# Kernel optimization log

Hardware: AMD Instinct MI355X
Metric: run time of the kernel (lower is better)

The kernel has to match this reference:

```python
import jax, jax.numpy as jnp
import numpy as np

N_ATOMS, E_ATOMS, E_BONDS, N_FRAGS, E_FRAGS = 200000, 800000, 3200000, 20000, 60000
D, EB, H, DH = 128, 12, 3, 4  # atom dim, bond-node feat dim, n_heads, per-head dim (EB // H)


def _seg_softmax(logits, seg, num):
    # scatter_softmax over segments given by `seg` along axis 0
    m = jax.ops.segment_max(logits, seg, num_segments=num)
    m = jnp.where(jnp.isfinite(m), m, 0.0)  # guard empty segments
    e = jnp.exp(logits - m[seg])
    s = jax.ops.segment_sum(e, seg, num_segments=num)
    return e / s[seg]


def setup_inputs() -> dict:
    key = jax.random.key(0)
    ks = jax.random.split(key, 16)
    s = 0.05
    return dict(
        x_atoms=jax.random.normal(ks[0], (N_ATOMS, D), jnp.float32),
        edge_index=jax.random.randint(ks[1], (2, E_ATOMS), 0, N_ATOMS, jnp.int32),
        edge_attr=jax.random.normal(ks[2], (E_ATOMS, EB), jnp.float32),
        frag_index=jax.random.randint(ks[3], (2, E_FRAGS), 0, N_FRAGS, jnp.int32),
        x_frags=jax.random.normal(ks[4], (N_FRAGS, D), jnp.float32),
        atom_to_frag_ids=jax.random.randint(ks[5], (N_ATOMS,), 0, N_FRAGS, jnp.int32),
        node_features_bond_graph=jax.random.normal(ks[6], (E_ATOMS, EB), jnp.float32),
        edge_index_bonds_graph=jax.random.randint(ks[7], (2, E_BONDS), 0, E_ATOMS, jnp.int32),
        edge_attr_bond_graph=jax.random.normal(ks[8], (E_BONDS, 1), jnp.float32),
        W_atom=jax.random.normal(ks[9], (D, D), jnp.float32) * s,
        b_atom=jnp.zeros((D,), jnp.float32),
        W_edge=jax.random.normal(ks[10], (EB, D), jnp.float32) * s,
        b_edge=jnp.zeros((D,), jnp.float32),
        W_proj=jax.random.normal(ks[11], (EB, EB), jnp.float32) * s,
        b_proj=jnp.zeros((EB,), jnp.float32),
        a_b=jax.random.normal(ks[12], (H, 2 * DH + 1), jnp.float32) * s,
        W_f1=jax.random.normal(ks[13], (D, 2 * D), jnp.float32) * s,
        b_f1=jnp.zeros((2 * D,), jnp.float32),
        W_f2=jax.random.normal(ks[14], (2 * D, D), jnp.float32) * s,
        b_f2=jnp.zeros((D,), jnp.float32),
    )


def reference(x_atoms, edge_index, edge_attr, frag_index, x_frags, atom_to_frag_ids,
              node_features_bond_graph, edge_index_bonds_graph, edge_attr_bond_graph,
              W_atom, b_atom, W_edge, b_edge, W_proj, b_proj, a_b,
              W_f1, b_f1, W_f2, b_f2):
    Nb = node_features_bond_graph.shape[0]  # bond-graph nodes == atom-graph edges
    N = x_atoms.shape[0]
    Nf = x_frags.shape[0]

    # ---- GAT-style attention on the bond (line) graph ----
    tgt_b, src_b = edge_index_bonds_graph[0], edge_index_bonds_graph[1]
    nf = (node_features_bond_graph @ W_proj + b_proj).reshape(Nb, H, DH)
    tf = nf[tgt_b]                                  # [Eb, H, DH]
    sf = nf[src_b]                                  # [Eb, H, DH]
    ea = jnp.broadcast_to(edge_attr_bond_graph[:, None, :], (tgt_b.shape[0], H, 1))
    msg = jnp.concatenate([tf, ea, sf], axis=-1)    # [Eb, H, 2*DH+1]
    logits = jax.nn.leaky_relu(jnp.sum(msg * a_b, axis=2), 0.2)  # [Eb, H]
    attn = _seg_softmax(logits, tgt_b, Nb)
    agg = jax.ops.segment_sum(attn[..., None] * sf, tgt_b, num_segments=Nb)  # [Nb, H, DH]
    new_bond = agg.reshape(Nb, H * DH)              # [Nb, EB]

    # edge embedding (computed in the original forward; not used in returned outputs)
    edge_attr_full = jnp.concatenate(
        [new_bond, jnp.zeros((N, EB), edge_attr.dtype)], axis=0)
    _ = edge_attr_full @ W_edge + b_edge

    # ---- degree-normalized GCN propagation on atom graph with self loops ----
    x = x_atoms @ W_atom + b_atom
    loop = jnp.arange(N, dtype=edge_index.dtype)
    src = jnp.concatenate([edge_index[0], loop])
    tgt = jnp.concatenate([edge_index[1], loop])
    deg = jax.ops.segment_sum(jnp.ones(src.shape, x.dtype), src, num_segments=N)
    dinv = jnp.where(deg > 0, 1.0 / jnp.sqrt(jnp.maximum(deg, 1.0)), 0.0)
    norm = dinv[src] * dinv[tgt]
    x_new = jax.ops.segment_sum(x[src] * norm[:, None], tgt, num_segments=N)  # [N, D]

    # ---- fragment pooling + fragment-graph propagation ----
    frag_feat = jax.ops.segment_sum(x_new, atom_to_frag_ids, num_segments=Nf)  # [Nf, D]
    fs, ft = frag_index[0], frag_index[1]
    frag_sum = jax.ops.segment_sum(frag_feat[fs], ft, num_segments=Nf)
    frag_out = jax.nn.relu(frag_sum @ W_f1 + b_f1) @ W_f2 + b_f2
    return (x_new, frag_out)
```

## Files before the change

kernel.cpp:

```cpp
#include <hip/hip_runtime.h>
#include <hip/hip_bf16.h>
#include <cstddef>

#define NA 200000
#define EA 800000
#define NF 20000
#define EF 60000
#define TOTW (EA + NA + EF)
#define CAPE 32
#define CAPA 64
#define CAPF 32
#define GRIDY (NA / 64)
#define LSTR 136

typedef unsigned short ushort_t;
typedef __attribute__((ext_vector_type(8))) short bf16x8;
typedef __attribute__((ext_vector_type(4))) float f32x4;

__device__ __forceinline__ unsigned short f2bf(float f) {
  unsigned u = __builtin_bit_cast(unsigned, f);
  u += 0x7FFFu + ((u >> 16) & 1u);
  return (unsigned short)(u >> 16);
}
__device__ __forceinline__ void acc2s(float& a, float& b, unsigned v, float s) {
  a = fmaf(__builtin_bit_cast(float, v << 16), s, a);
  b = fmaf(__builtin_bit_cast(float, v & 0xFFFF0000u), s, b);
}

__global__ __launch_bounds__(256) void k_wt(const float* __restrict__ W,
                                            ushort_t* __restrict__ Wt) {
  int idx = blockIdx.x * 256 + threadIdx.x;
  if (idx < 128 * 128) {
    int c = idx >> 7, k = idx & 127;
    Wt[idx] = f2bf(W[k * 128 + c]);
  }
}

__global__ __launch_bounds__(256) void k_fused(
    const int* __restrict__ ei, const int* __restrict__ a2f,
    const int* __restrict__ fi, int* __restrict__ cnt_src,
    int* __restrict__ cnt_e, int* __restrict__ cnt_a, int* __restrict__ cnt_f,
    int* __restrict__ lst_e, int* __restrict__ lst_a, int* __restrict__ lst_f,
    const float* __restrict__ xa, const ushort_t* __restrict__ Wt,
    const float* __restrict__ b, ushort_t* __restrict__ y) {
  __shared__ ushort_t Asl[64 * LSTR];
  __shared__ ushort_t Bsl[128 * LSTR];
  const int tid = threadIdx.x;
  const int brow = blockIdx.x * 64;

  for (int idx = blockIdx.x * 256 + tid; idx < TOTW; idx += GRIDY * 256) {
    if (idx < EA) {
      int s = ei[idx], t = ei[EA + idx];
      atomicAdd(&cnt_src[s], 1);
      int p = atomicAdd(&cnt_e[t], 1);
      if (p < CAPE) lst_e[t * CAPE + p] = s;
    } else if (idx < EA + NA) {
      int i = idx - EA;
      int f = a2f[i];
      int p = atomicAdd(&cnt_a[f], 1);
      if (p < CAPA) lst_a[f * CAPA + p] = i;
    } else {
      int e = idx - EA - NA;
      int p = atomicAdd(&cnt_f[fi[EF + e]], 1);
      if (p < CAPF) lst_f[fi[EF + e] * CAPF + p] = fi[e];
    }
  }

  {
    const float4* gA = reinterpret_cast<const float4*>(xa + (size_t)brow * 128);
#pragma unroll
    for (int i = 0; i < 8; ++i) {
      int f = tid + i * 256;
      int row = f >> 5;
      int kq = f & 31;
      float4 v = gA[f];
      ushort4 u;
      u.x = f2bf(v.x); u.y = f2bf(v.y); u.z = f2bf(v.z); u.w = f2bf(v.w);
      int off = (((kq >> 2) & 1) << 2) | ((kq & 3) << 3) | ((kq >> 3) << 5);
      *reinterpret_cast<ushort4*>(&Asl[row * LSTR + off]) = u;
    }
    const uint4* gW = reinterpret_cast<const uint4*>(Wt);
#pragma unroll
    for (int i = 0; i < 8; ++i) {
      int uix = tid + i * 256;
      int c = uix >> 4;
      int k8 = uix & 15;
      uint4 v = gW[uix];
      int base0 = ((k8 & 2) << 1) | ((k8 & 1) << 4) | ((k8 >> 2) << 5);
      uint2 lo, hi;
      lo.x = v.x; lo.y = v.y;
      hi.x = v.z; hi.y = v.w;
      *reinterpret_cast<uint2*>(&Bsl[c * LSTR + base0]) = lo;
      *reinterpret_cast<uint2*>(&Bsl[c * LSTR + base0 + 8]) = hi;
    }
  }
  __syncthreads();
  const int w = tid >> 6;
  const int l = tid & 63;
  const int lr = l & 15;
  const int g = l >> 4;
  const int r0 = w * 16;
  f32x4 acc[8] = {};
  const int arow = r0 + lr;
#pragma unroll
  for (int s = 0; s < 4; ++s) {
    const int foff = g * 8 + s * 32;
    bf16x8 a = *reinterpret_cast<const bf16x8*>(&Asl[arow * LSTR + foff]);
#pragma unroll
    for (int t = 0; t < 8; ++t) {
      bf16x8 bf = *reinterpret_cast<const bf16x8*>(&Bsl[(t * 16 + lr) * LSTR + foff]);
      acc[t] = __builtin_amdgcn_mfma_f32_16x16x32_bf16(a, bf, acc[t], 0, 0, 0);
    }
  }
#pragma unroll
  for (int t = 0; t < 8; ++t) {
    const int col = t * 16 + lr;
    const float bb = b[col];
#pragma unroll
    for (int r = 0; r < 4; ++r) {
      const int row = brow + r0 + g * 4 + r;
      y[(size_t)row * 128 + col] = f2bf(acc[t][r] + bb);
    }
  }
}

__global__ __launch_bounds__(256) void k_gather_x(
    const int* __restrict__ cnt_e, const int* __restrict__ lst_e,
    const ushort_t* __restrict__ y, const int* __restrict__ cnt_src,
    float* __restrict__ xnew) {
  const int row = blockIdx.x * 16 + (threadIdx.x >> 4);
  const int lane = threadIdx.x & 15;
  const int c0 = lane * 8;
  const float dt = rsqrtf(1.0f + (float)cnt_src[row]);
  float a0 = 0, a1 = 0, a2 = 0, a3 = 0, a4 = 0, a5 = 0, a6 = 0, a7 = 0;
  {
    uint4 v = *reinterpret_cast<const uint4*>(y + (size_t)row * 128 + c0);
    acc2s(a0, a1, v.x, dt); acc2s(a2, a3, v.y, dt);
    acc2s(a4, a5, v.z, dt); acc2s(a6, a7, v.w, dt);
  }
  const int base = row * CAPE;
  int deg = cnt_e[row];
  deg = (deg < CAPE) ? deg : CAPE;
  int j = 0;
  for (; j + 4 <= deg; j += 4) {
    const int s0 = lst_e[base + j + 0];
    const int s1 = lst_e[base + j + 1];
    const int s2 = lst_e[base + j + 2];
    const int s3 = lst_e[base + j + 3];
    const float d0 = rsqrtf(1.0f + (float)cnt_src[s0]);
    const float d1 = rsqrtf(1.0f + (float)cnt_src[s1]);
    const float d2 = rsqrtf(1.0f + (float)cnt_src[s2]);
    const float d3 = rsqrtf(1.0f + (float)cnt_src[s3]);
    const uint4 w0 = *reinterpret_cast<const uint4*>(y + (size_t)s0 * 128 + c0);
    const uint4 w1 = *reinterpret_cast<const uint4*>(y + (size_t)s1 * 128 + c0);
    const uint4 w2 = *reinterpret_cast<const uint4*>(y + (size_t)s2 * 128 + c0);
    const uint4 w3 = *reinterpret_cast<const uint4*>(y + (size_t)s3 * 128 + c0);
    acc2s(a0, a1, w0.x, d0); acc2s(a2, a3, w0.y, d0); acc2s(a4, a5, w0.z, d0); acc2s(a6, a7, w0.w, d0);
    acc2s(a0, a1, w1.x, d1); acc2s(a2, a3, w1.y, d1); acc2s(a4, a5, w1.z, d1); acc2s(a6, a7, w1.w, d1);
    acc2s(a0, a1, w2.x, d2); acc2s(a2, a3, w2.y, d2); acc2s(a4, a5, w2.z, d2); acc2s(a6, a7, w2.w, d2);
    acc2s(a0, a1, w3.x, d3); acc2s(a2, a3, w3.y, d3); acc2s(a4, a5, w3.z, d3); acc2s(a6, a7, w3.w, d3);
  }
  for (; j < deg; ++j) {
    const int s = lst_e[base + j];
    const float dn = rsqrtf(1.0f + (float)cnt_src[s]);
    const uint4 w = *reinterpret_cast<const uint4*>(y + (size_t)s * 128 + c0);
    acc2s(a0, a1, w.x, dn); acc2s(a2, a3, w.y, dn);
    acc2s(a4, a5, w.z, dn); acc2s(a6, a7, w.w, dn);
  }
  f32x4 q0 = {a0 * dt, a1 * dt, a2 * dt, a3 * dt};
  f32x4 q1 = {a4 * dt, a5 * dt, a6 * dt, a7 * dt};
  float* o = xnew + (size_t)row * 128 + c0;
  __builtin_nontemporal_store(q0, reinterpret_cast<f32x4*>(o));
  __builtin_nontemporal_store(q1, reinterpret_cast<f32x4*>(o + 4));
}

__global__ __launch_bounds__(256) void k_gather_ff(
    const int* __restrict__ cnt_a, const int* __restrict__ lst_a,
    const float* __restrict__ xnew, float* __restrict__ ff) {
  const int f = blockIdx.x * 8 + (threadIdx.x >> 5);
  const int c = (threadIdx.x & 31) << 2;
  float4 acc = {0.f, 0.f, 0.f, 0.f};
  const int base = f * CAPA;
  int deg = cnt_a[f];
  deg = (deg < CAPA) ? deg : CAPA;
  int j = 0;
  for (; j + 4 <= deg; j += 4) {
    const int s0 = lst_a[base + j + 0];
    const int s1 = lst_a[base + j + 1];
    const int s2 = lst_a[base + j + 2];
    const int s3 = lst_a[base + j + 3];
    const float4 v0 = *reinterpret_cast<const float4*>(xnew + (size_t)s0 * 128 + c);
    const float4 v1 = *reinterpret_cast<const float4*>(xnew + (size_t)s1 * 128 + c);
    const float4 v2 = *reinterpret_cast<const float4*>(xnew + (size_t)s2 * 128 + c);
    const float4 v3 = *reinterpret_cast<const float4*>(xnew + (size_t)s3 * 128 + c);
    acc.x += v0.x + v1.x + v2.x + v3.x;
    acc.y += v0.y + v1.y + v2.y + v3.y;
    acc.z += v0.z + v1.z + v2.z + v3.z;
    acc.w += v0.w + v1.w + v2.w + v3.w;
  }
  for (; j < deg; ++j) {
    const int s = lst_a[base + j];
    const float4 v = *reinterpret_cast<const float4*>(xnew + (size_t)s * 128 + c);
    acc.x += v.x; acc.y += v.y; acc.z += v.z; acc.w += v.w;
  }
  *reinterpret_cast<float4*>(ff + (size_t)f * 128 + c) = acc;
}

__global__ __launch_bounds__(256) void k_mlp(
    const int* __restrict__ cnt_f, const int* __restrict__ lst_f,
    const float* __restrict__ ff,
    const float* __restrict__ W1, const float* __restrict__ b1,
    const float* __restrict__ W2, const float* __restrict__ b2,
    float* __restrict__ out) {
  __shared__ float As[32][128];
  __shared__ float hs[32][256];
  const int row0 = blockIdx.x * 32;
  {
    const int g = threadIdx.x >> 5;
    const int c = (threadIdx.x & 31) << 2;
#pragma unroll
    for (int rr = 0; rr < 4; ++rr) {
      const int f = row0 + g * 4 + rr;
      const int base = f * CAPF;
      int deg = cnt_f[f];
      deg = (deg < CAPF) ? deg : CAPF;
      float4 acc = {0.f, 0.f, 0.f, 0.f};
      for (int j = 0; j < deg; ++j) {
        const int s = lst_f[base + j];
        const float4 v = *reinterpret_cast<const float4*>(ff + (size_t)s * 128 + c);
        acc.x += v.x; acc.y += v.y; acc.z += v.z; acc.w += v.w;
      }
      *reinterpret_cast<float4*>(&As[g * 4 + rr][c]) = acc;
    }
  }
  __syncthreads();
  {
    const int tc = threadIdx.x & 63;
    const int tr = threadIdx.x >> 6;
    const int c0 = tc * 4;
    float acc[8][4] = {};
    for (int k0 = 0; k0 < 128; k0 += 4) {
      float4 w0 = *reinterpret_cast<const float4*>(&W1[(k0 + 0) * 256 + c0]);
      float4 w1 = *reinterpret_cast<const float4*>(&W1[(k0 + 1) * 256 + c0]);
      float4 w2 = *reinterpret_cast<const float4*>(&W1[(k0 + 2) * 256 + c0]);
      float4 w3 = *reinterpret_cast<const float4*>(&W1[(k0 + 3) * 256 + c0]);
#pragma unroll
      for (int r = 0; r < 8; ++r) {
        float4 a = *reinterpret_cast<const float4*>(&As[tr * 8 + r][k0]);
        acc[r][0] += a.x * w0.x + a.y * w1.x + a.z * w2.x + a.w * w3.x;
        acc[r][1] += a.x * w0.y + a.y * w1.y + a.z * w2.y + a.w * w3.y;
        acc[r][2] += a.x * w0.z + a.y * w1.z + a.z * w2.z + a.w * w3.z;
        acc[r][3] += a.x * w0.w + a.y * w1.w + a.z * w2.w + a.w * w3.w;
      }
    }
    const float4 bc = *reinterpret_cast<const float4*>(&b1[c0]);
#pragma unroll
    for (int r = 0; r < 8; ++r) {
      float4 h;
      h.x = fmaxf(acc[r][0] + bc.x, 0.f);
      h.y = fmaxf(acc[r][1] + bc.y, 0.f);
      h.z = fmaxf(acc[r][2] + bc.z, 0.f);
      h.w = fmaxf(acc[r][3] + bc.w, 0.f);
      *reinterpret_cast<float4*>(&hs[tr * 8 + r][c0]) = h;
    }
  }
  __syncthreads();
  {
    const int tc = threadIdx.x & 31;
    const int tr = threadIdx.x >> 5;
    const int c0 = tc * 4;
    float acc[4][4] = {};
    for (int k0 = 0; k0 < 256; k0 += 4) {
      float4 w0 = *reinterpret_cast<const float4*>(&W2[(k0 + 0) * 128 + c0]);
      float4 w1 = *reinterpret_cast<const float4*>(&W2[(k0 + 1) * 128 + c0]);
      float4 w2 = *reinterpret_cast<const float4*>(&W2[(k0 + 2) * 128 + c0]);
      float4 w3 = *reinterpret_cast<const float4*>(&W2[(k0 + 3) * 128 + c0]);
#pragma unroll
      for (int r = 0; r < 4; ++r) {
        float4 a = *reinterpret_cast<const float4*>(&hs[tr * 4 + r][k0]);
        acc[r][0] += a.x * w0.x + a.y * w1.x + a.z * w2.x + a.w * w3.x;
        acc[r][1] += a.x * w0.y + a.y * w1.y + a.z * w2.y + a.w * w3.y;
        acc[r][2] += a.x * w0.z + a.y * w1.z + a.z * w2.z + a.w * w3.z;
        acc[r][3] += a.x * w0.w + a.y * w1.w + a.z * w2.w + a.w * w3.w;
      }
    }
    const float4 bc = *reinterpret_cast<const float4*>(&b2[c0]);
#pragma unroll
    for (int r = 0; r < 4; ++r) {
      float4 o;
      o.x = acc[r][0] + bc.x;
      o.y = acc[r][1] + bc.y;
      o.z = acc[r][2] + bc.z;
      o.w = acc[r][3] + bc.w;
      *reinterpret_cast<float4*>(&out[(size_t)(row0 + tr * 4 + r) * 128 + c0]) = o;
    }
  }
}

extern "C" void kernel_launch(void* const* d_in, const int* in_sizes, int n_in,
                              void* d_out, int out_size, void* d_ws, size_t ws_size,
                              hipStream_t stream) {
  const float* x_atoms    = (const float*)d_in[0];
  const int*   edge_index = (const int*)d_in[1];
  const int*   frag_index = (const int*)d_in[3];
  const int*   a2f        = (const int*)d_in[5];
  const float* W_atom     = (const float*)d_in[9];
  const float* b_atom     = (const float*)d_in[10];
  const float* W_f1       = (const float*)d_in[16];
  const float* b_f1       = (const float*)d_in[17];
  const float* W_f2       = (const float*)d_in[18];
  const float* b_f2       = (const float*)d_in[19];

  char* ws = (char*)d_ws;
  size_t off = 0;
  auto alloc = [&](size_t bytes) {
    void* p = ws + off;
    off += (bytes + 255) & ~(size_t)255;
    return p;
  };
  int* cnt_src = (int*)alloc((size_t)NA * 4);
  int* cnt_e   = (int*)alloc((size_t)NA * 4);
  int* cnt_a   = (int*)alloc((size_t)NF * 4);
  int* cnt_f   = (int*)alloc((size_t)NF * 4);
  const size_t zero_bytes = off;
  int* lst_e   = (int*)alloc((size_t)NA * CAPE * 4);
  int* lst_a   = (int*)alloc((size_t)NF * CAPA * 4);
  int* lst_f   = (int*)alloc((size_t)NF * CAPF * 4);
  ushort_t* Wt = (ushort_t*)alloc((size_t)128 * 128 * 2);
  ushort_t* y  = (ushort_t*)alloc((size_t)NA * 128 * 2);
  float* ff    = (float*)alloc((size_t)NF * 128 * 4);

  float* xnew = (float*)d_out;
  float* fout = (float*)d_out + (size_t)NA * 128;

  (void)hipMemsetAsync(ws, 0, zero_bytes, stream);

  k_wt<<<64, 256, 0, stream>>>(W_atom, Wt);
  k_fused<<<GRIDY, 256, 0, stream>>>(edge_index, a2f, frag_index,
                                     cnt_src, cnt_e, cnt_a, cnt_f,
                                     lst_e, lst_a, lst_f,
                                     x_atoms, Wt, b_atom, y);
  k_gather_x<<<NA / 16, 256, 0, stream>>>(cnt_e, lst_e, y, cnt_src, xnew);
  k_gather_ff<<<NF / 8, 256, 0, stream>>>(cnt_a, lst_a, xnew, ff);
  k_mlp     <<<NF / 32, 256, 0, stream>>>(cnt_f, lst_f, ff, W_f1, b_f1,
                                          W_f2, b_f2, fout);
}
```

Baseline: 269.2 us.

## Stage GEMM operands in K-chunks to shrink LDS footprint in fused kernel

The fused kernel no longer loads the full 64x128 A tile and 128x128 B tile into LDS at once. It now loads 32-wide K slices per step into buffers of stride 40, syncing between steps. This cuts LDS use from about 52KB to about 15KB per block, which should let more blocks stay resident and overlap the atomic-heavy list-building phase. The cost is four barrier rounds instead of one, plus smaller, less coalesced global loads per step, with no double buffering.

New measurement: 276.3 us. 2.6% more time.

```diff
diff --git a/kernel.cpp b/kernel.cpp
--- a/kernel.cpp
+++ b/kernel.cpp
@@ -11,7 +11,7 @@
 #define CAPA 64
 #define CAPF 32
 #define GRIDY (NA / 64)
-#define LSTR 136
+#define CSTR 40
 
 typedef unsigned short ushort_t;
 typedef __attribute__((ext_vector_type(8))) short bf16x8;
@@ -43,8 +43,8 @@
     int* __restrict__ lst_e, int* __restrict__ lst_a, int* __restrict__ lst_f,
     const float* __restrict__ xa, const ushort_t* __restrict__ Wt,
     const float* __restrict__ b, ushort_t* __restrict__ y) {
-  __shared__ ushort_t Asl[64 * LSTR];
-  __shared__ ushort_t Bsl[128 * LSTR];
+  __shared__ ushort_t Asl[64 * CSTR];
+  __shared__ ushort_t Bsl[128 * CSTR];
   const int tid = threadIdx.x;
   const int brow = blockIdx.x * 64;
 
@@ -66,49 +66,49 @@
     }
   }
 
-  {
-    const float4* gA = reinterpret_cast<const float4*>(xa + (size_t)brow * 128);
-#pragma unroll
-    for (int i = 0; i < 8; ++i) {
-      int f = tid + i * 256;
-      int row = f >> 5;
-      int kq = f & 31;
-      float4 v = gA[f];
-      ushort4 u;
-      u.x = f2bf(v.x); u.y = f2bf(v.y); u.z = f2bf(v.z); u.w = f2bf(v.w);
-      int off = (((kq >> 2) & 1) << 2) | ((kq & 3) << 3) | ((kq >> 3) << 5);
-      *reinterpret_cast<ushort4*>(&Asl[row * LSTR + off]) = u;
-    }
-    const uint4* gW = reinterpret_cast<const uint4*>(Wt);
-#pragma unroll
-    for (int i = 0; i < 8; ++i) {
-      int uix = tid + i * 256;
-      int c = uix >> 4;
-      int k8 = uix & 15;
-      uint4 v = gW[uix];
-      int base0 = ((k8 & 2) << 1) | ((k8 & 1) << 4) | ((k8 >> 2) << 5);
-      uint2 lo, hi;
-      lo.x = v.x; lo.y = v.y;
-      hi.x = v.z; hi.y = v.w;
-      *reinterpret_cast<uint2*>(&Bsl[c * LSTR + base0]) = lo;
-      *reinterpret_cast<uint2*>(&Bsl[c * LSTR + base0 + 8]) = hi;
-    }
-  }
-  __syncthreads();
   const int w = tid >> 6;
   const int l = tid & 63;
   const int lr = l & 15;
   const int g = l >> 4;
   const int r0 = w * 16;
+  const int arow = r0 + lr;
   f32x4 acc[8] = {};
-  const int arow = r0 + lr;
 #pragma unroll
   for (int s = 0; s < 4; ++s) {
-    const int foff = g * 8 + s * 32;
-    bf16x8 a = *reinterpret_cast<const bf16x8*>(&Asl[arow * LSTR + foff]);
+    if (s > 0) __syncthreads();
+    {
+      const float4* gA = reinterpret_cast<const float4*>(xa + (size_t)brow * 128);
+#pragma unroll
+      for (int i = 0; i < 2; ++i) {
+        int f = tid + i * 256;
+        int row = f >> 3;
+        int kq = f & 7;
+        float4 v = gA[row * 32 + s * 8 + kq];
+        ushort4 u;
+        u.x = f2bf(v.x); u.y = f2bf(v.y); u.z = f2bf(v.z); u.w = f2bf(v.w);
+        int off = ((kq & 3) << 3) | ((kq >> 2) << 2);
+        *reinterpret_cast<ushort4*>(&Asl[row * CSTR + off]) = u;
+      }
+      const uint4* gW = reinterpret_cast<const uint4*>(Wt);
+#pragma unroll
+      for (int i = 0; i < 2; ++i) {
+        int f = tid + i * 256;
+        int c = f >> 2;
+        int k8 = f & 3;
+        uint4 v = gW[c * 16 + s * 4 + k8];
+        int base0 = ((k8 & 1) << 4) | ((k8 >> 1) << 2);
+        uint2 lo, hi;
+        lo.x = v.x; lo.y = v.y;
+        hi.x = v.z; hi.y = v.w;
+        *reinterpret_cast<uint2*>(&Bsl[c * CSTR + base0]) = lo;
+        *reinterpret_cast<uint2*>(&Bsl[c * CSTR + base0 + 8]) = hi;
+      }
+    }
+    __syncthreads();
+    bf16x8 a = *reinterpret_cast<const bf16x8*>(&Asl[arow * CSTR + g * 8]);
 #pragma unroll
     for (int t = 0; t < 8; ++t) {
-      bf16x8 bf = *reinterpret_cast<const bf16x8*>(&Bsl[(t * 16 + lr) * LSTR + foff]);
+      bf16x8 bf = *reinterpret_cast<const bf16x8*>(&Bsl[(t * 16 + lr) * CSTR + g * 8]);
       acc[t] = __builtin_amdgcn_mfma_f32_16x16x32_bf16(a, bf, acc[t], 0, 0, 0);
     }
   }
```
